# Performance work log

Measured on AMD Instinct MI355X. Metric: run time of the kernel, lower is better.

## Reference

```python
import jax, jax.numpy as jnp
import numpy as np

K = 2
N_NODES = 100_000
N_EDGES = 1_600_000
STATIC_F = 16
DYN_F = 32
EDGE_F = 8
IN_F = EDGE_F + 2 * STATIC_F + 2 * DYN_F  # 104
HID_F = 2 * DYN_F  # 64


def setup_inputs() -> dict:
    key = jax.random.key(0)
    ks = jax.random.split(key, 9)
    x_s = jax.random.normal(ks[0], (N_NODES, STATIC_F), dtype=jnp.float32)
    x_t = jax.random.normal(ks[1], (N_NODES, DYN_F), dtype=jnp.float32)
    edge_index = jax.random.randint(ks[2], (2, N_EDGES), 0, N_NODES, dtype=jnp.int64 if jax.config.jax_enable_x64 else jnp.int32)
    edge_attr = jax.random.normal(ks[3], (N_EDGES, EDGE_F), dtype=jnp.float32)
    W1 = jax.random.normal(ks[4], (IN_F, HID_F), dtype=jnp.float32) / np.sqrt(IN_F)
    b1 = jnp.zeros((HID_F,), dtype=jnp.float32)
    W2 = jax.random.normal(ks[5], (HID_F, DYN_F), dtype=jnp.float32) / np.sqrt(HID_F)
    b2 = jnp.zeros((DYN_F,), dtype=jnp.float32)
    F = jax.random.normal(ks[6], (K + 1, DYN_F, DYN_F), dtype=jnp.float32) / np.sqrt(DYN_F)
    return {"x_s": x_s, "x_t": x_t, "edge_index": edge_index, "edge_attr": edge_attr,
            "W1": W1, "b1": b1, "W2": W2, "b2": b2, "F": F}


def reference(x_s, x_t, edge_index, edge_attr, W1, b1, W2, b2, F):
    row, col = edge_index[0], edge_index[1]
    num_nodes = x_t.shape[0]
    # filter_matrix[0] (Linear, no bias); F[k] stored as [in, out]
    out = x_t @ F[0]
    xs_row = x_s[row]  # static gathers are loop-invariant
    xs_col = x_s[col]
    for k in range(K):
        mask = jnp.sum(out, axis=1) != 0  # [N]
        edge_mask = (mask[row] | mask[col]).astype(out.dtype)[:, None]  # [E,1]
        out_row = out[row]
        out_col = out[col]
        e_ij = jnp.concatenate([xs_row, xs_col, out_row, out_col, edge_attr], axis=1)  # [E,104]
        w_ij = jax.nn.relu(e_ij @ W1 + b1) @ W2 + b2  # [E,32]
        # normalize per edge; NaN (zero-norm) -> 0, matching masked_fill_
        nrm = jnp.linalg.norm(w_ij, axis=1, keepdims=True)
        w_ij = jnp.where(nrm > 0, w_ij / jnp.where(nrm > 0, nrm, 1.0), 0.0)
        # with_gradient: (x_j - x_i) * w_ij; zero out edges failing the mask
        shift = (out_col - out_row) * w_ij * edge_mask
        scattered = jax.ops.segment_sum(shift, col, num_segments=num_nodes)
        out = out + scattered @ F[k + 1]
    return out
```

## Files before the change

### kernel.cpp

```cpp
#include <hip/hip_runtime.h>

#define NN 100000
#define NE 1600000
#define SF 16
#define DF 32
#define EFT 8
#define HF 64

typedef __attribute__((ext_vector_type(8))) _Float16 half8;
typedef __attribute__((ext_vector_type(4))) _Float16 half4v;
typedef __attribute__((ext_vector_type(8))) short short8;
typedef __attribute__((ext_vector_type(4))) float floatx4;

__device__ inline int hswz(int row, int halfoff) {
  int gran = halfoff >> 3, sub = halfoff & 7;
  return row * 64 + ((gran ^ (row & 7)) << 3) + sub;
}

__global__ __launch_bounds__(256) void hist_kernel(const int* __restrict__ ei,
                                                   int* __restrict__ deg) {
  int e = blockIdx.x * 256 + threadIdx.x;
  if (e < NE) atomicAdd(&deg[ei[NE + e]], 1);
}

__global__ __launch_bounds__(256) void scan1_kernel(const int* __restrict__ deg,
                                                    int* __restrict__ cur,
                                                    int* __restrict__ bsums) {
  __shared__ int ts[256];
  int tid = threadIdx.x;
  int base = blockIdx.x * 1024 + tid * 4;
  int v[4];
#pragma unroll
  for (int q = 0; q < 4; ++q) v[q] = (base + q < NN) ? deg[base + q] : 0;
  int s = v[0] + v[1] + v[2] + v[3];
  ts[tid] = s;
  __syncthreads();
  for (int off = 1; off < 256; off <<= 1) {
    int t = (tid >= off) ? ts[tid - off] : 0;
    __syncthreads();
    ts[tid] += t;
    __syncthreads();
  }
  int excl = ts[tid] - s;
  if (tid == 255) bsums[blockIdx.x] = ts[255];
  int run = excl;
#pragma unroll
  for (int q = 0; q < 4; ++q) {
    if (base + q < NN) cur[base + q] = run;
    run += v[q];
  }
}

__global__ __launch_bounds__(256) void scan3_kernel(int* __restrict__ cur,
                                                    const int* __restrict__ bsums) {
  int i = blockIdx.x * 256 + threadIdx.x;
  int g = blockIdx.x >> 2;
  int pref = 0;
  for (int q = 0; q < g; ++q) pref += bsums[q];
  if (i < NN) cur[i] += pref;
}

__global__ __launch_bounds__(256) void setup_kernel(
    const float* __restrict__ W1, const float* __restrict__ W2,
    _Float16* __restrict__ WpreT, _Float16* __restrict__ w2pk,
    _Float16* __restrict__ w1epk,
    float4* __restrict__ scattered4, int* __restrict__ deg) {
  int gid = blockIdx.x * 256 + threadIdx.x;
  if (gid < 800000) {
    float4 z = {0.f, 0.f, 0.f, 0.f};
    scattered4[gid] = z;
  }
  if (gid < NN) deg[gid] = 0;
  if (gid < 128 * 64) {
    int col = gid >> 6, k = gid & 63;
    int j = col & 63;
    bool bh = col >= 64;
    float v = 0.f;
    if (k < 16) v = W1[((bh ? 16 : 0) + k) * HF + j];
    else if (k < 48) v = W1[((bh ? 64 : 32) + (k - 16)) * HF + j];
    WpreT[gid] = (_Float16)v;
  }
  if (gid < 2048) {
    int lane = gid >> 5, idx = gid & 31;
    int kt = idx >> 4, nt = (idx >> 3) & 1, q = idx & 7;
    int kgrp = (lane >> 4) & 3, lcol = lane & 15;
    w2pk[gid] = (_Float16)W2[(kt * 32 + kgrp * 8 + q) * DF + nt * 16 + lcol];
  } else if (gid < 4096) {
    int id = gid - 2048;
    int lane = id >> 5, idx = id & 31;
    int jblk = idx >> 3, t = idx & 7;
    float v = (lane < 16) ? W1[(96 + t) * HF + jblk * 16 + lane] : 0.f;
    w1epk[id] = (_Float16)v;
  }
}

__global__ __launch_bounds__(256) void fill_kernel(
    const int* __restrict__ ei, const float* __restrict__ ea,
    int* __restrict__ cur, char* __restrict__ recs) {
  int e = blockIdx.x * 256 + threadIdx.x;
  int r = ei[e];
  int c = ei[NE + e];
  int pos = atomicAdd(&cur[c], 1);
  const float4* p = (const float4*)(ea + (size_t)e * EFT);
  float4 v0 = p[0], v1 = p[1];
  union { _Float16 h[2]; int i; } p01, p23, p45, p67;
  p01.h[0] = (_Float16)v0.x; p01.h[1] = (_Float16)v0.y;
  p23.h[0] = (_Float16)v0.z; p23.h[1] = (_Float16)v0.w;
  p45.h[0] = (_Float16)v1.x; p45.h[1] = (_Float16)v1.y;
  p67.h[0] = (_Float16)v1.z; p67.h[1] = (_Float16)v1.w;
  int2* rp = (int2*)(recs + (size_t)pos * 24);
  int2 a = {r, c};
  int2 b = {p01.i, p23.i};
  int2 d = {p45.i, p67.i};
  rp[0] = a; rp[1] = b; rp[2] = d;
}

__global__ __launch_bounds__(256) void init_kernel(
    const float* __restrict__ x_t, const float* __restrict__ F0,
    float* __restrict__ out, _Float16* __restrict__ outb,
    float* __restrict__ sums) {
  int n = blockIdx.x * 256 + threadIdx.x;
  if (n >= NN) return;
  float x[DF];
  const float4* xr = reinterpret_cast<const float4*>(x_t + (size_t)n * DF);
#pragma unroll
  for (int q = 0; q < 8; ++q) {
    float4 v = xr[q];
    x[4*q+0]=v.x; x[4*q+1]=v.y; x[4*q+2]=v.z; x[4*q+3]=v.w;
  }
  float4* orow = reinterpret_cast<float4*>(out + (size_t)n * DF);
  _Float16* ob = outb + (size_t)n * DF;
  float s = 0.f;
#pragma unroll
  for (int q = 0; q < 8; ++q) {
    float4 acc = {0.f, 0.f, 0.f, 0.f};
#pragma unroll
    for (int i = 0; i < DF; ++i) {
      float xi = x[i];
      acc.x = fmaf(xi, F0[i*DF + 4*q+0], acc.x);
      acc.y = fmaf(xi, F0[i*DF + 4*q+1], acc.y);
      acc.z = fmaf(xi, F0[i*DF + 4*q+2], acc.z);
      acc.w = fmaf(xi, F0[i*DF + 4*q+3], acc.w);
    }
    orow[q] = acc;
    s += acc.x + acc.y + acc.z + acc.w;
    half4v pk = {(_Float16)acc.x, (_Float16)acc.y, (_Float16)acc.z, (_Float16)acc.w};
    *(half4v*)(ob + 4*q) = pk;
  }
  sums[n] = s;
}

__global__ __launch_bounds__(256, 4) void pre_kernel(
    const float* __restrict__ x_s, const _Float16* __restrict__ outb,
    const _Float16* __restrict__ WpreT, _Float16* __restrict__ ABh) {
  __shared__ _Float16 wlds[128][72];
  int tid = threadIdx.x;
  for (int t = tid; t < 1024; t += 256) {
    int colr = t >> 3, kc = t & 7;
    *(half8*)(&wlds[colr][kc * 8]) = *(const half8*)(WpreT + colr * 64 + kc * 8);
  }
  __syncthreads();

  int lcol = tid & 15, kgrp = (tid >> 4) & 3, wid = tid >> 6;
  int nodebase = blockIdx.x * 64 + wid * 16;
  int nodeA = nodebase + lcol;

  half8 a0 = {}, a1 = {};
  if (nodeA < NN) {
    const _Float16* obp = outb + (size_t)nodeA * DF;
    if (kgrp < 2) {
      const float4* p = (const float4*)(x_s + (size_t)nodeA * SF);
      float4 v0 = p[kgrp * 2], v1 = p[kgrp * 2 + 1];
      a0[0]=(_Float16)v0.x; a0[1]=(_Float16)v0.y;
      a0[2]=(_Float16)v0.z; a0[3]=(_Float16)v0.w;
      a0[4]=(_Float16)v1.x; a0[5]=(_Float16)v1.y;
      a0[6]=(_Float16)v1.z; a0[7]=(_Float16)v1.w;
      a1 = *(const half8*)(obp + 16 + kgrp * 8);
    } else if (kgrp == 2) {
      a0 = *(const half8*)(obp + 0);
    } else {
      a0 = *(const half8*)(obp + 8);
    }
  }

  floatx4 acc[8];
#pragma unroll
  for (int nt = 0; nt < 8; ++nt) {
    half8 b0 = *(const half8*)(&wlds[nt * 16 + lcol][kgrp * 8]);
    half8 b1v = *(const half8*)(&wlds[nt * 16 + lcol][32 + kgrp * 8]);
    floatx4 c = {0.f, 0.f, 0.f, 0.f};
    c = __builtin_amdgcn_mfma_f32_16x16x32_f16(a0, b0, c, 0, 0, 0);
    c = __builtin_amdgcn_mfma_f32_16x16x32_f16(a1, b1v, c, 0, 0, 0);
    acc[nt] = c;
  }

#pragma unroll
  for (int rr = 0; rr < 4; ++rr) {
    int node = nodebase + kgrp * 4 + rr;
    if (node < NN) {
      _Float16* dst = ABh + (size_t)node * 128;
#pragma unroll
      for (int nt = 0; nt < 8; ++nt)
        dst[nt * 16 + lcol] = (_Float16)acc[nt][rr];
    }
  }
}

__global__ __launch_bounds__(256, 4) void edge_kernel(
    const _Float16* __restrict__ ABh, const _Float16* __restrict__ outb,
    const float* __restrict__ sums, const char* __restrict__ recs,
    const float* __restrict__ b1, const float* __restrict__ b2,
    const _Float16* __restrict__ w2pk, const _Float16* __restrict__ w1epk,
    float* __restrict__ scattered) {
  __shared__ union { _Float16 h[256 * 64]; float sh[256 * 33]; } u;
  __shared__ int scol[256];
  __shared__ unsigned short l0[256], l1[256];
  __shared__ int wbase[4];
  __shared__ int cnt;

  int tid = threadIdx.x;
  int bbase = blockIdx.x * 256;
  int i = bbase + tid;
  if (tid == 0) cnt = 0;
  int lcol = tid & 15, kgrp = (tid >> 4) & 3, wid = tid >> 6;
  int lane = tid & 63;

  const int2* rp = (const int2*)(recs + (size_t)i * 24);
  int2 ra = rp[0], rb = rp[1], rd = rp[2];
  int r = ra.x;
  int c = ra.y;
  int4 eai = {rb.x, rb.y, rd.x, rd.y};
  scol[tid] = c;
  float s_r = sums[r], s_c = sums[c];

  half8 Ar[8], Bc[8];
  {
    const half8* arp = (const half8*)(ABh + (size_t)r * 128);
    const half8* bcp = (const half8*)(ABh + (size_t)c * 128 + 64);
#pragma unroll
    for (int q = 0; q < 8; ++q) { Ar[q] = arp[q]; Bc[q] = bcp[q]; }
  }

  float b2c0 = b2[lcol], b2c1 = b2[16 + lcol];

  const _Float16* wep = w1epk + (size_t)lane * 32;
  half8 wA0 = *(const half8*)(wep);
  half8 wA1 = *(const half8*)(wep + 8);
  half8 wA2 = *(const half8*)(wep + 16);
  half8 wA3 = *(const half8*)(wep + 24);
  const float4* b1f4 = (const float4*)b1;
  float4 b1q0 = b1f4[0 + kgrp];
  float4 b1q1 = b1f4[4 + kgrp];
  float4 b1q2 = b1f4[8 + kgrp];
  float4 b1q3 = b1f4[12 + kgrp];
  bool lo16 = lane < 16;
#pragma unroll
  for (int g = 0; g < 4; ++g) {
    int src = g * 16 + lcol;
    int4 t;
    t.x = __shfl(eai.x, src, 64);
    t.y = __shfl(eai.y, src, 64);
    t.z = __shfl(eai.z, src, 64);
    t.w = __shfl(eai.w, src, 64);
    half8 zz = {};
    half8 bg = lo16 ? __builtin_bit_cast(half8, t) : zz;
    int erow = wid * 64 + g * 16 + lcol;
    {
      floatx4 cc = {b1q0.x, b1q0.y, b1q0.z, b1q0.w};
      cc = __builtin_amdgcn_mfma_f32_16x16x32_f16(wA0, bg, cc, 0, 0, 0);
      half4v h4 = {(_Float16)cc[0], (_Float16)cc[1], (_Float16)cc[2], (_Float16)cc[3]};
      *(half4v*)(&u.h[hswz(erow, 0 * 16 + kgrp * 4)]) = h4;
    }
    {
      floatx4 cc = {b1q1.x, b1q1.y, b1q1.z, b1q1.w};
      cc = __builtin_amdgcn_mfma_f32_16x16x32_f16(wA1, bg, cc, 0, 0, 0);
      half4v h4 = {(_Float16)cc[0], (_Float16)cc[1], (_Float16)cc[2], (_Float16)cc[3]};
      *(half4v*)(&u.h[hswz(erow, 1 * 16 + kgrp * 4)]) = h4;
    }
    {
      floatx4 cc = {b1q2.x, b1q2.y, b1q2.z, b1q2.w};
      cc = __builtin_amdgcn_mfma_f32_16x16x32_f16(wA2, bg, cc, 0, 0, 0);
      half4v h4 = {(_Float16)cc[0], (_Float16)cc[1], (_Float16)cc[2], (_Float16)cc[3]};
      *(half4v*)(&u.h[hswz(erow, 2 * 16 + kgrp * 4)]) = h4;
    }
    {
      floatx4 cc = {b1q3.x, b1q3.y, b1q3.z, b1q3.w};
      cc = __builtin_amdgcn_mfma_f32_16x16x32_f16(wA3, bg, cc, 0, 0, 0);
      half4v h4 = {(_Float16)cc[0], (_Float16)cc[1], (_Float16)cc[2], (_Float16)cc[3]};
      *(half4v*)(&u.h[hswz(erow, 3 * 16 + kgrp * 4)]) = h4;
    }
  }

#pragma unroll
  for (int q = 0; q < 8; ++q) {
    int idx = hswz(tid, q * 8);
    half8 w = *(const half8*)(&u.h[idx]);
    half8 s = Ar[q] + Bc[q] + w;
    short8 sb = __builtin_bit_cast(short8, s);
    short8 m = sb >> 15;
    sb = sb & ~m;
    *(short8*)(&u.h[idx]) = sb;
  }

  const _Float16* wpp = w2pk + (size_t)lane * 32;
  half8 w2f00 = *(const half8*)(wpp);
  half8 w2f01 = *(const half8*)(wpp + 8);
  half8 w2f10 = *(const half8*)(wpp + 16);
  half8 w2f11 = *(const half8*)(wpp + 24);
  floatx4 acc[4][2];
#pragma unroll
  for (int g = 0; g < 4; ++g) {
    int erow = wid * 64 + g * 16 + lcol;
    half8 a0 = *(const half8*)(&u.h[hswz(erow, kgrp * 8)]);
    half8 a1 = *(const half8*)(&u.h[hswz(erow, 32 + kgrp * 8)]);
    floatx4 c0 = {b2c0, b2c0, b2c0, b2c0};
    floatx4 c1 = {b2c1, b2c1, b2c1, b2c1};
    c0 = __builtin_amdgcn_mfma_f32_16x16x32_f16(a0, w2f00, c0, 0, 0, 0);
    c0 = __builtin_amdgcn_mfma_f32_16x16x32_f16(a1, w2f10, c0, 0, 0, 0);
    c1 = __builtin_amdgcn_mfma_f32_16x16x32_f16(a0, w2f01, c1, 0, 0, 0);
    c1 = __builtin_amdgcn_mfma_f32_16x16x32_f16(a1, w2f11, c1, 0, 0, 0);
    acc[g][0] = c0;
    acc[g][1] = c1;
  }

  half8 Or[4], Oc[4];
  {
    const half8* orp = (const half8*)(outb + (size_t)r * DF);
    const half8* ocp = (const half8*)(outb + (size_t)c * DF);
#pragma unroll
    for (int q = 0; q < 4; ++q) { Or[q] = orp[q]; Oc[q] = ocp[q]; }
  }

  __syncthreads();

#pragma unroll
  for (int g = 0; g < 4; ++g) {
#pragma unroll
    for (int rr = 0; rr < 4; ++rr) {
      int e = wid * 64 + g * 16 + kgrp * 4 + rr;
      u.sh[e * 33 + lcol]      = acc[g][0][rr];
      u.sh[e * 33 + 16 + lcol] = acc[g][1][rr];
    }
  }

  {
    float o2[32];
    float nsq = 0.f;
#pragma unroll
    for (int j = 0; j < 32; ++j) {
      float v = u.sh[tid * 33 + j];
      o2[j] = v;
      nsq = fmaf(v, v, nsq);
    }
    float ms = (nsq > 0.f) ? rsqrtf(nsq) : 0.f;
    if (s_r == 0.f && s_c == 0.f) ms = 0.f;
#pragma unroll
    for (int q = 0; q < 4; ++q) {
#pragma unroll
      for (int jj = 0; jj < 8; ++jj)
        u.sh[tid * 33 + q * 8 + jj] =
            ((float)Oc[q][jj] - (float)Or[q][jj]) * o2[q * 8 + jj] * ms;
    }
  }
  __syncthreads();

  int c_self = scol[tid];
  bool head = (tid == 0 || scol[tid - 1] != c_self);
  unsigned long long m = __ballot(head);
  if (lane == 0) wbase[wid] = atomicAdd(&cnt, (int)__popcll(m));
  __syncthreads();
  if (head) {
    int idx = wbase[wid] + (int)__popcll(m & ((1ull << lane) - 1ull));
    int t1 = tid + 1;
    while (t1 < 256 && scol[t1] == c_self) ++t1;
    l0[idx] = (unsigned short)tid;
    l1[idx] = (unsigned short)t1;
  }
  __syncthreads();
  int nr = cnt;
  for (int task = tid; task < nr * 32; task += 256) {
    int rid = task >> 5, j = task & 31;
    int t0 = l0[rid], t1 = l1[rid];
    float s = 0.f;
    for (int t = t0; t < t1; ++t) s += u.sh[t * 33 + j];
    unsafeAtomicAdd(&scattered[(size_t)scol[t0] * DF + j], s);
  }
}

__global__ __launch_bounds__(256) void node_kernel(
    float* __restrict__ out, float* __restrict__ scattered,
    const float* __restrict__ Fk, _Float16* __restrict__ outb,
    float* __restrict__ sums) {
  int n = blockIdx.x * 256 + threadIdx.x;
  if (n >= NN) return;
  float s[DF];
  float4* sp = reinterpret_cast<float4*>(scattered + (size_t)n * DF);
#pragma unroll
  for (int q = 0; q < 8; ++q) {
    float4 v = sp[q];
    s[4*q+0]=v.x; s[4*q+1]=v.y; s[4*q+2]=v.z; s[4*q+3]=v.w;
  }
  float4* op = reinterpret_cast<float4*>(out + (size_t)n * DF);
  _Float16* ob = outb + (size_t)n * DF;
  float ssum = 0.f;
#pragma unroll
  for (int q = 0; q < 8; ++q) {
    float4 acc = op[q];
#pragma unroll
    for (int i = 0; i < DF; ++i) {
      float si = s[i];
      acc.x = fmaf(si, Fk[i*DF + 4*q+0], acc.x);
      acc.y = fmaf(si, Fk[i*DF + 4*q+1], acc.y);
      acc.z = fmaf(si, Fk[i*DF + 4*q+2], acc.z);
      acc.w = fmaf(si, Fk[i*DF + 4*q+3], acc.w);
    }
    op[q] = acc;
    ssum += acc.x + acc.y + acc.z + acc.w;
    half4v pk = {(_Float16)acc.x, (_Float16)acc.y, (_Float16)acc.z, (_Float16)acc.w};
    *(half4v*)(ob + 4*q) = pk;
  }
  sums[n] = ssum;
  float4 z = {0.f, 0.f, 0.f, 0.f};
#pragma unroll
  for (int q = 0; q < 8; ++q) sp[q] = z;
}

extern "C" void kernel_launch(void* const* d_in, const int* in_sizes, int n_in,
                              void* d_out, int out_size, void* d_ws, size_t ws_size,
                              hipStream_t stream) {
  const float* x_s = (const float*)d_in[0];
  const float* x_t = (const float*)d_in[1];
  const int*   ei  = (const int*)d_in[2];
  const float* ea  = (const float*)d_in[3];
  const float* W1  = (const float*)d_in[4];
  const float* b1  = (const float*)d_in[5];
  const float* W2  = (const float*)d_in[6];
  const float* b2  = (const float*)d_in[7];
  const float* F   = (const float*)d_in[8];

  float* out = (float*)d_out;
  char* ws = (char*)d_ws;
  float*     scattered = (float*)(ws);
  _Float16*  ABh       = (_Float16*)(ws + 12800000);
  _Float16*  outb      = (_Float16*)(ws + 38400000);
  float*     sums      = (float*)(ws + 44800000);
  char*      recs      = (char*)(ws + 45200000);
  int*       deg       = (int*)(ws + 83600000);
  int*       cur       = (int*)(ws + 84000000);
  int*       bsums     = (int*)(ws + 84400000);
  _Float16*  WpreT     = (_Float16*)(ws + 84410000);
  _Float16*  w2pk      = (_Float16*)(ws + 84430000);
  _Float16*  w1epk     = (_Float16*)(ws + 84440000);

  dim3 blk(256);
  dim3 grid_e(NE / 256);
  dim3 grid_n((NN + 255) / 256);
  dim3 grid_p((NN + 63) / 64);
  int nscan = (NN + 1023) / 1024;

  setup_kernel<<<3125, blk, 0, stream>>>(W1, W2, WpreT, w2pk, w1epk,
                                         (float4*)scattered, deg);
  hist_kernel<<<grid_e, blk, 0, stream>>>(ei, deg);
  scan1_kernel<<<nscan, blk, 0, stream>>>(deg, cur, bsums);
  scan3_kernel<<<grid_n, blk, 0, stream>>>(cur, bsums);
  fill_kernel<<<grid_e, blk, 0, stream>>>(ei, ea, cur, recs);

  init_kernel<<<grid_n, blk, 0, stream>>>(x_t, F, out, outb, sums);

  for (int k = 0; k < 2; ++k) {
    pre_kernel<<<grid_p, blk, 0, stream>>>(x_s, outb, WpreT, ABh);
    edge_kernel<<<grid_e, blk, 0, stream>>>(ABh, outb, sums, recs, b1, b2,
                                            w2pk, w1epk, scattered);
    node_kernel<<<grid_n, blk, 0, stream>>>(out, scattered,
                                            F + (size_t)(k + 1) * DF * DF,
                                            outb, sums);
  }
}
```

Measured before the change: 441.8 us.

## Fuse node update with per-node precompute and fold histogram into setup

Merges the init and node-update kernels with the following pre_kernel, passing the fresh fp16 node rows through shared memory instead of re-reading them from global. It also spreads each node's 32x32 update across four threads, folds the degree histogram into the setup kernel (with a memset to clear deg), and uses a lighter final node kernel that skips the fp16 and sums writes. Together this removes several launches and some global round-trips. The cost is extra shared memory per block and fewer nodes per thread.

```diff
diff --git a/kernel.cpp b/kernel.cpp
--- a/kernel.cpp
+++ b/kernel.cpp
@@ -15,12 +15,6 @@
 __device__ inline int hswz(int row, int halfoff) {
   int gran = halfoff >> 3, sub = halfoff & 7;
   return row * 64 + ((gran ^ (row & 7)) << 3) + sub;
-}
-
-__global__ __launch_bounds__(256) void hist_kernel(const int* __restrict__ ei,
-                                                   int* __restrict__ deg) {
-  int e = blockIdx.x * 256 + threadIdx.x;
-  if (e < NE) atomicAdd(&deg[ei[NE + e]], 1);
 }
 
 __global__ __launch_bounds__(256) void scan1_kernel(const int* __restrict__ deg,
@@ -61,6 +55,7 @@
 }
 
 __global__ __launch_bounds__(256) void setup_kernel(
+    const int* __restrict__ ei,
     const float* __restrict__ W1, const float* __restrict__ W2,
     _Float16* __restrict__ WpreT, _Float16* __restrict__ w2pk,
     _Float16* __restrict__ w1epk,
@@ -70,7 +65,6 @@
     float4 z = {0.f, 0.f, 0.f, 0.f};
     scattered4[gid] = z;
   }
-  if (gid < NN) deg[gid] = 0;
   if (gid < 128 * 64) {
     int col = gid >> 6, k = gid & 63;
     int j = col & 63;
@@ -92,6 +86,7 @@
     float v = (lane < 16) ? W1[(96 + t) * HF + jblk * 16 + lane] : 0.f;
     w1epk[id] = (_Float16)v;
   }
+  atomicAdd(&deg[ei[NE + gid]], 1);
 }
 
 __global__ __launch_bounds__(256) void fill_kernel(
@@ -115,59 +110,18 @@
   rp[0] = a; rp[1] = b; rp[2] = d;
 }
 
-__global__ __launch_bounds__(256) void init_kernel(
-    const float* __restrict__ x_t, const float* __restrict__ F0,
-    float* __restrict__ out, _Float16* __restrict__ outb,
-    float* __restrict__ sums) {
-  int n = blockIdx.x * 256 + threadIdx.x;
-  if (n >= NN) return;
-  float x[DF];
-  const float4* xr = reinterpret_cast<const float4*>(x_t + (size_t)n * DF);
-#pragma unroll
-  for (int q = 0; q < 8; ++q) {
-    float4 v = xr[q];
-    x[4*q+0]=v.x; x[4*q+1]=v.y; x[4*q+2]=v.z; x[4*q+3]=v.w;
-  }
-  float4* orow = reinterpret_cast<float4*>(out + (size_t)n * DF);
-  _Float16* ob = outb + (size_t)n * DF;
-  float s = 0.f;
-#pragma unroll
-  for (int q = 0; q < 8; ++q) {
-    float4 acc = {0.f, 0.f, 0.f, 0.f};
-#pragma unroll
-    for (int i = 0; i < DF; ++i) {
-      float xi = x[i];
-      acc.x = fmaf(xi, F0[i*DF + 4*q+0], acc.x);
-      acc.y = fmaf(xi, F0[i*DF + 4*q+1], acc.y);
-      acc.z = fmaf(xi, F0[i*DF + 4*q+2], acc.z);
-      acc.w = fmaf(xi, F0[i*DF + 4*q+3], acc.w);
-    }
-    orow[q] = acc;
-    s += acc.x + acc.y + acc.z + acc.w;
-    half4v pk = {(_Float16)acc.x, (_Float16)acc.y, (_Float16)acc.z, (_Float16)acc.w};
-    *(half4v*)(ob + 4*q) = pk;
-  }
-  sums[n] = s;
-}
-
-__global__ __launch_bounds__(256, 4) void pre_kernel(
-    const float* __restrict__ x_s, const _Float16* __restrict__ outb,
-    const _Float16* __restrict__ WpreT, _Float16* __restrict__ ABh) {
-  __shared__ _Float16 wlds[128][72];
-  int tid = threadIdx.x;
-  for (int t = tid; t < 1024; t += 256) {
-    int colr = t >> 3, kc = t & 7;
-    *(half8*)(&wlds[colr][kc * 8]) = *(const half8*)(WpreT + colr * 64 + kc * 8);
-  }
-  __syncthreads();
-
+__device__ inline void pre_body(int tid, int bbase64,
+                                const float* __restrict__ x_s,
+                                const _Float16 (*wlds)[72],
+                                const _Float16 (*obs)[32],
+                                _Float16* __restrict__ ABh) {
   int lcol = tid & 15, kgrp = (tid >> 4) & 3, wid = tid >> 6;
-  int nodebase = blockIdx.x * 64 + wid * 16;
+  int nodebase = bbase64 + wid * 16;
   int nodeA = nodebase + lcol;
+  int ln = wid * 16 + lcol;
 
   half8 a0 = {}, a1 = {};
   if (nodeA < NN) {
-    const _Float16* obp = outb + (size_t)nodeA * DF;
     if (kgrp < 2) {
       const float4* p = (const float4*)(x_s + (size_t)nodeA * SF);
       float4 v0 = p[kgrp * 2], v1 = p[kgrp * 2 + 1];
@@ -175,11 +129,11 @@
       a0[2]=(_Float16)v0.z; a0[3]=(_Float16)v0.w;
       a0[4]=(_Float16)v1.x; a0[5]=(_Float16)v1.y;
       a0[6]=(_Float16)v1.z; a0[7]=(_Float16)v1.w;
-      a1 = *(const half8*)(obp + 16 + kgrp * 8);
+      a1 = *(const half8*)(&obs[ln][16 + kgrp * 8]);
     } else if (kgrp == 2) {
-      a0 = *(const half8*)(obp + 0);
+      a0 = *(const half8*)(&obs[ln][0]);
     } else {
-      a0 = *(const half8*)(obp + 8);
+      a0 = *(const half8*)(&obs[ln][8]);
     }
   }
 
@@ -204,6 +158,120 @@
         dst[nt * 16 + lcol] = (_Float16)acc[nt][rr];
     }
   }
+}
+
+__global__ __launch_bounds__(256) void initpre_kernel(
+    const float* __restrict__ x_t, const float* __restrict__ F0,
+    const float* __restrict__ x_s, const _Float16* __restrict__ WpreT,
+    float* __restrict__ out, _Float16* __restrict__ outb,
+    float* __restrict__ sums, _Float16* __restrict__ ABh) {
+  __shared__ _Float16 wlds[128][72];
+  __shared__ _Float16 obs[64][32];
+  int tid = threadIdx.x;
+  for (int t = tid; t < 1024; t += 256) {
+    int colr = t >> 3, kc = t & 7;
+    *(half8*)(&wlds[colr][kc * 8]) = *(const half8*)(WpreT + colr * 64 + kc * 8);
+  }
+
+  int nl = tid >> 2, q = tid & 3;
+  int node = blockIdx.x * 64 + nl;
+  if (node < NN) {
+    float o[8];
+#pragma unroll
+    for (int jj = 0; jj < 8; ++jj) o[jj] = 0.f;
+    const float4* xt4 = (const float4*)(x_t + (size_t)node * DF);
+#pragma unroll
+    for (int it = 0; it < 8; ++it) {
+      float4 xv = xt4[it];
+#pragma unroll
+      for (int k = 0; k < 4; ++k) {
+        float xk = (k == 0) ? xv.x : (k == 1) ? xv.y : (k == 2) ? xv.z : xv.w;
+        const float* frow = F0 + (it * 4 + k) * DF + q * 8;
+        float4 f0 = *(const float4*)(frow);
+        float4 f1 = *(const float4*)(frow + 4);
+        o[0] = fmaf(xk, f0.x, o[0]); o[1] = fmaf(xk, f0.y, o[1]);
+        o[2] = fmaf(xk, f0.z, o[2]); o[3] = fmaf(xk, f0.w, o[3]);
+        o[4] = fmaf(xk, f1.x, o[4]); o[5] = fmaf(xk, f1.y, o[5]);
+        o[6] = fmaf(xk, f1.z, o[6]); o[7] = fmaf(xk, f1.w, o[7]);
+      }
+    }
+    float4* op = (float4*)(out + (size_t)node * DF + q * 8);
+    float4 w0 = {o[0], o[1], o[2], o[3]};
+    float4 w1 = {o[4], o[5], o[6], o[7]};
+    op[0] = w0; op[1] = w1;
+    half8 pk;
+#pragma unroll
+    for (int jj = 0; jj < 8; ++jj) pk[jj] = (_Float16)o[jj];
+    *(half8*)(outb + (size_t)node * DF + q * 8) = pk;
+    *(half8*)(&obs[nl][q * 8]) = pk;
+    float s = o[0]+o[1]+o[2]+o[3]+o[4]+o[5]+o[6]+o[7];
+    s += __shfl_xor(s, 1, 64);
+    s += __shfl_xor(s, 2, 64);
+    if (q == 0) sums[node] = s;
+  }
+  __syncthreads();
+  pre_body(tid, blockIdx.x * 64, x_s, wlds, obs, ABh);
+}
+
+__global__ __launch_bounds__(256) void nodepre_kernel(
+    float* __restrict__ out, float* __restrict__ scattered,
+    const float* __restrict__ Fk,
+    const float* __restrict__ x_s, const _Float16* __restrict__ WpreT,
+    _Float16* __restrict__ outb, float* __restrict__ sums,
+    _Float16* __restrict__ ABh) {
+  __shared__ _Float16 wlds[128][72];
+  __shared__ _Float16 obs[64][32];
+  int tid = threadIdx.x;
+  for (int t = tid; t < 1024; t += 256) {
+    int colr = t >> 3, kc = t & 7;
+    *(half8*)(&wlds[colr][kc * 8]) = *(const half8*)(WpreT + colr * 64 + kc * 8);
+  }
+
+  int nl = tid >> 2, q = tid & 3;
+  int node = blockIdx.x * 64 + nl;
+  if (node < NN) {
+    float o[8];
+    {
+      const float4* op4 = (const float4*)(out + (size_t)node * DF + q * 8);
+      float4 b0 = op4[0], b1 = op4[1];
+      o[0]=b0.x; o[1]=b0.y; o[2]=b0.z; o[3]=b0.w;
+      o[4]=b1.x; o[5]=b1.y; o[6]=b1.z; o[7]=b1.w;
+    }
+    const float4* sc4 = (const float4*)(scattered + (size_t)node * DF);
+#pragma unroll
+    for (int it = 0; it < 8; ++it) {
+      float4 sv = sc4[it];
+#pragma unroll
+      for (int k = 0; k < 4; ++k) {
+        float sk = (k == 0) ? sv.x : (k == 1) ? sv.y : (k == 2) ? sv.z : sv.w;
+        const float* frow = Fk + (it * 4 + k) * DF + q * 8;
+        float4 f0 = *(const float4*)(frow);
+        float4 f1 = *(const float4*)(frow + 4);
+        o[0] = fmaf(sk, f0.x, o[0]); o[1] = fmaf(sk, f0.y, o[1]);
+        o[2] = fmaf(sk, f0.z, o[2]); o[3] = fmaf(sk, f0.w, o[3]);
+        o[4] = fmaf(sk, f1.x, o[4]); o[5] = fmaf(sk, f1.y, o[5]);
+        o[6] = fmaf(sk, f1.z, o[6]); o[7] = fmaf(sk, f1.w, o[7]);
+      }
+    }
+    float4* op = (float4*)(out + (size_t)node * DF + q * 8);
+    float4 w0 = {o[0], o[1], o[2], o[3]};
+    float4 w1 = {o[4], o[5], o[6], o[7]};
+    op[0] = w0; op[1] = w1;
+    half8 pk;
+#pragma unroll
+    for (int jj = 0; jj < 8; ++jj) pk[jj] = (_Float16)o[jj];
+    *(half8*)(outb + (size_t)node * DF + q * 8) = pk;
+    *(half8*)(&obs[nl][q * 8]) = pk;
+    float s = o[0]+o[1]+o[2]+o[3]+o[4]+o[5]+o[6]+o[7];
+    s += __shfl_xor(s, 1, 64);
+    s += __shfl_xor(s, 2, 64);
+    if (q == 0) sums[node] = s;
+    float4 z = {0.f, 0.f, 0.f, 0.f};
+    float4* zp = (float4*)(scattered + (size_t)node * DF + q * 8);
+    zp[0] = z; zp[1] = z;
+  }
+  __syncthreads();
+  pre_body(tid, blockIdx.x * 64, x_s, wlds, obs, ABh);
 }
 
 __global__ __launch_bounds__(256, 4) void edge_kernel(
@@ -387,22 +455,19 @@
   }
 }
 
-__global__ __launch_bounds__(256) void node_kernel(
-    float* __restrict__ out, float* __restrict__ scattered,
-    const float* __restrict__ Fk, _Float16* __restrict__ outb,
-    float* __restrict__ sums) {
+__global__ __launch_bounds__(256) void node_final_kernel(
+    float* __restrict__ out, const float* __restrict__ scattered,
+    const float* __restrict__ Fk) {
   int n = blockIdx.x * 256 + threadIdx.x;
   if (n >= NN) return;
   float s[DF];
-  float4* sp = reinterpret_cast<float4*>(scattered + (size_t)n * DF);
+  const float4* sp = reinterpret_cast<const float4*>(scattered + (size_t)n * DF);
 #pragma unroll
   for (int q = 0; q < 8; ++q) {
     float4 v = sp[q];
     s[4*q+0]=v.x; s[4*q+1]=v.y; s[4*q+2]=v.z; s[4*q+3]=v.w;
   }
   float4* op = reinterpret_cast<float4*>(out + (size_t)n * DF);
-  _Float16* ob = outb + (size_t)n * DF;
-  float ssum = 0.f;
 #pragma unroll
   for (int q = 0; q < 8; ++q) {
     float4 acc = op[q];
@@ -415,14 +480,7 @@
       acc.w = fmaf(si, Fk[i*DF + 4*q+3], acc.w);
     }
     op[q] = acc;
-    ssum += acc.x + acc.y + acc.z + acc.w;
-    half4v pk = {(_Float16)acc.x, (_Float16)acc.y, (_Float16)acc.z, (_Float16)acc.w};
-    *(half4v*)(ob + 4*q) = pk;
-  }
-  sums[n] = ssum;
-  float4 z = {0.f, 0.f, 0.f, 0.f};
-#pragma unroll
-  for (int q = 0; q < 8; ++q) sp[q] = z;
+  }
 }
 
 extern "C" void kernel_launch(void* const* d_in, const int* in_sizes, int n_in,
@@ -458,21 +516,22 @@
   dim3 grid_p((NN + 63) / 64);
   int nscan = (NN + 1023) / 1024;
 
-  setup_kernel<<<3125, blk, 0, stream>>>(W1, W2, WpreT, w2pk, w1epk,
-                                         (float4*)scattered, deg);
-  hist_kernel<<<grid_e, blk, 0, stream>>>(ei, deg);
+  hipMemsetAsync(deg, 0, NN * sizeof(int), stream);
+  setup_kernel<<<grid_e, blk, 0, stream>>>(ei, W1, W2, WpreT, w2pk, w1epk,
+                                           (float4*)scattered, deg);
   scan1_kernel<<<nscan, blk, 0, stream>>>(deg, cur, bsums);
   scan3_kernel<<<grid_n, blk, 0, stream>>>(cur, bsums);
   fill_kernel<<<grid_e, blk, 0, stream>>>(ei, ea, cur, recs);
 
-  init_kernel<<<grid_n, blk, 0, stream>>>(x_t, F, out, outb, sums);
-
-  for (int k = 0; k < 2; ++k) {
-    pre_kernel<<<grid_p, blk, 0, stream>>>(x_s, outb, WpreT, ABh);
-    edge_kernel<<<grid_e, blk, 0, stream>>>(ABh, outb, sums, recs, b1, b2,
-                                            w2pk, w1epk, scattered);
-    node_kernel<<<grid_n, blk, 0, stream>>>(out, scattered,
-                                            F + (size_t)(k + 1) * DF * DF,
-                                            outb, sums);
-  }
-}
+  initpre_kernel<<<grid_p, blk, 0, stream>>>(x_t, F, x_s, WpreT,
+                                             out, outb, sums, ABh);
+  edge_kernel<<<grid_e, blk, 0, stream>>>(ABh, outb, sums, recs, b1, b2,
+                                          w2pk, w1epk, scattered);
+  nodepre_kernel<<<grid_p, blk, 0, stream>>>(out, scattered,
+                                             F + (size_t)1 * DF * DF,
+                                             x_s, WpreT, outb, sums, ABh);
+  edge_kernel<<<grid_e, blk, 0, stream>>>(ABh, outb, sums, recs, b1, b2,
+                                          w2pk, w1epk, scattered);
+  node_final_kernel<<<grid_n, blk, 0, stream>>>(out, scattered,
+                                                F + (size_t)2 * DF * DF);
+}
```

New measurement: 431.6 us. 2.3% less time.
